# Kernel tuning notes

Hardware: AMD Instinct MI355X
Metric: run time of the kernel (lower is better)

Reference implementation:

```python
import jax, jax.numpy as jnp
import numpy as np

D_DIM = 100000  # vocabulary size
W_DIM = 128     # embedding width
BATCH = 4096    # number of (center, context) index pairs


def setup_inputs() -> dict:
    key = jax.random.key(0)
    k1, k2, kw1, kb1, kw2, kb2 = jax.random.split(key, 6)
    idx1 = jax.random.randint(k1, (BATCH,), 0, D_DIM, dtype=jnp.int64 if jax.config.jax_enable_x64 else jnp.int32)
    idx2 = jax.random.randint(k2, (BATCH,), 0, D_DIM, dtype=jnp.int64 if jax.config.jax_enable_x64 else jnp.int32)
    # torch.nn.Linear(D, W): weight [W, D], bias [W], uniform(-1/sqrt(D), 1/sqrt(D))
    bound = 1.0 / np.sqrt(D_DIM)
    W1 = jax.random.uniform(kw1, (W_DIM, D_DIM), jnp.float32, -bound, bound)
    b1 = jax.random.uniform(kb1, (W_DIM,), jnp.float32, -bound, bound)
    W2 = jax.random.uniform(kw2, (W_DIM, D_DIM), jnp.float32, -bound, bound)
    b2 = jax.random.uniform(kb2, (W_DIM,), jnp.float32, -bound, bound)
    return {"idx1": idx1, "idx2": idx2, "W1": W1, "b1": b1, "W2": W2, "b2": b2}


def reference(idx1, idx2, W1, b1, W2, b2):
    # Linear(one_hot(idx)) == weight[:, idx] + bias  -> direct row (column) gather.
    p1 = W1[:, idx1].T + b1              # [B, W_dim]
    p2 = W2[:, idx2].T + b2              # [B, W_dim]
    s = jax.nn.sigmoid(jnp.sum(p1 * p2, axis=-1))  # [B]
    # original: cat([1 - sigmoid, sigmoid]) -> [B, 2]
    return jnp.stack([1.0 - s, s], axis=-1)
```

## Files before the change

kernel.cpp:

```cpp
#include <hip/hip_runtime.h>
#include <math.h>

#define D_DIM 100000
#define W_DIM 128
#define BATCH 4096

__global__ __launch_bounds__(256) void sgns_kernel(
    const int* __restrict__ idx1,
    const int* __restrict__ idx2,
    const float* __restrict__ W1,
    const float* __restrict__ b1,
    const float* __restrict__ W2,
    const float* __restrict__ b2,
    float* __restrict__ out)
{
    const int gtid = blockIdx.x * blockDim.x + threadIdx.x;
    const int wave = gtid >> 6;
    const int lane = gtid & 63;
    if (wave >= BATCH) return;

    const int i1 = idx1[wave];
    const int i2 = idx2[wave];

    const int w0 = lane;
    const int w1 = lane + 64;

    const float a0 = W1[w0 * D_DIM + i1];
    const float a1 = W1[w1 * D_DIM + i1];
    const float c0 = W2[w0 * D_DIM + i2];
    const float c1 = W2[w1 * D_DIM + i2];

    const float p0 = a0 + b1[w0];
    const float p1 = a1 + b1[w1];
    const float q0 = c0 + b2[w0];
    const float q1 = c1 + b2[w1];

    float v = p0 * q0 + p1 * q1;

    #pragma unroll
    for (int off = 32; off > 0; off >>= 1)
        v += __shfl_down(v, off, 64);

    if (lane == 0) {
        const float s = 1.0f / (1.0f + expf(-v));
        out[wave * 2 + 0] = 1.0f - s;
        out[wave * 2 + 1] = s;
    }
}

extern "C" void kernel_launch(void* const* d_in, const int* in_sizes, int n_in,
                              void* d_out, int out_size, void* d_ws, size_t ws_size,
                              hipStream_t stream)
{
    const int*   idx1 = (const int*)  d_in[0];
    const int*   idx2 = (const int*)  d_in[1];
    const float* W1   = (const float*)d_in[2];
    const float* b1   = (const float*)d_in[3];
    const float* W2   = (const float*)d_in[4];
    const float* b2   = (const float*)d_in[5];
    float* out = (float*)d_out;

    const int threads = 256;
    const int blocks  = (BATCH * 64) / threads;
    sgns_kernel<<<blocks, threads, 0, stream>>>(idx1, idx2, W1, b1, W2, b2, out);
}
```

Baseline: 125.2 us.

## Gather embedding columns via inverse-index scatter so reads coalesce across vocabulary

Replaces the per-pair strided column gather with a four-kernel pipeline. It first initialises inverse-index maps, then uses atomicMin to map each vocabulary id to the first batch position that uses it. Next, threads indexed by vocabulary id copy the needed columns into compact row-major buffers, so adjacent threads read adjacent addresses. A final kernel computes the dot products from those buffers. This targets the uncoalesced 4-byte reads with 400KB stride, but adds three extra launches, workspace traffic, and a gather pass that scans all 100k ids per table.

```diff
diff --git a/kernel.cpp b/kernel.cpp
--- a/kernel.cpp
+++ b/kernel.cpp
@@ -4,38 +4,86 @@
 #define D_DIM 100000
 #define W_DIM 128
 #define BATCH 4096
+#define NOREP 0x7FFFFFFF
 
-__global__ __launch_bounds__(256) void sgns_kernel(
-    const int* __restrict__ idx1,
-    const int* __restrict__ idx2,
-    const float* __restrict__ W1,
-    const float* __restrict__ b1,
-    const float* __restrict__ W2,
-    const float* __restrict__ b2,
-    float* __restrict__ out)
+
+__global__ __launch_bounds__(256) void k_init(int* __restrict__ inv)
+{
+    const int t = blockIdx.x * 256 + threadIdx.x;
+    if (t < (2 * D_DIM) / 4)
+        reinterpret_cast<int4*>(inv)[t] = make_int4(NOREP, NOREP, NOREP, NOREP);
+}
+
+__global__ __launch_bounds__(256) void k_scatter(const int* __restrict__ idx1,
+                                                 const int* __restrict__ idx2,
+                                                 int* __restrict__ inv1,
+                                                 int* __restrict__ inv2)
+{
+    const int b = blockIdx.x * 256 + threadIdx.x;
+    if (b < BATCH) {
+        atomicMin(&inv1[idx1[b]], b);
+        atomicMin(&inv2[idx2[b]], b);
+    }
+}
+
+__global__ __launch_bounds__(256) void k_gather(const float* __restrict__ W1,
+                                                const float* __restrict__ W2,
+                                                const int*   __restrict__ inv1,
+                                                const int*   __restrict__ inv2,
+                                                float* __restrict__ p1,
+                                                float* __restrict__ p2)
+{
+    const float* __restrict__ W   = blockIdx.y ? W2   : W1;
+    const int*   __restrict__ inv = blockIdx.y ? inv2 : inv1;
+    float*       __restrict__ p   = blockIdx.y ? p2   : p1;
+
+    const int i = blockIdx.x * 256 + threadIdx.x;
+    if (i >= D_DIM) return;
+    const int j = inv[i];
+    if (j == NOREP) return;
+
+    const float* __restrict__ src = W + i;
+    float*       __restrict__ dst = p + j * W_DIM;
+    #pragma unroll 8
+    for (int w = 0; w < W_DIM; ++w)
+        dst[w] = src[w * D_DIM];
+}
+
+__global__ __launch_bounds__(256) void k_dot(const int* __restrict__ idx1,
+                                             const int* __restrict__ idx2,
+                                             const int* __restrict__ inv1,
+                                             const int* __restrict__ inv2,
+                                             const float* __restrict__ p1,
+                                             const float* __restrict__ p2,
+                                             const float* __restrict__ b1,
+                                             const float* __restrict__ b2,
+                                             float* __restrict__ out)
 {
     const int gtid = blockIdx.x * blockDim.x + threadIdx.x;
     const int wave = gtid >> 6;
     const int lane = gtid & 63;
     if (wave >= BATCH) return;
 
-    const int i1 = idx1[wave];
-    const int i2 = idx2[wave];
+    const int r1 = inv1[idx1[wave]];
+    const int r2 = inv2[idx2[wave]];
+
+    const float* __restrict__ P1 = p1 + r1 * W_DIM;
+    const float* __restrict__ P2 = p2 + r2 * W_DIM;
 
     const int w0 = lane;
     const int w1 = lane + 64;
 
-    const float a0 = W1[w0 * D_DIM + i1];
-    const float a1 = W1[w1 * D_DIM + i1];
-    const float c0 = W2[w0 * D_DIM + i2];
-    const float c1 = W2[w1 * D_DIM + i2];
+    const float a0 = P1[w0];
+    const float a1 = P1[w1];
+    const float c0 = P2[w0];
+    const float c1 = P2[w1];
 
-    const float p0 = a0 + b1[w0];
-    const float p1 = a1 + b1[w1];
-    const float q0 = c0 + b2[w0];
-    const float q1 = c1 + b2[w1];
+    const float x0 = a0 + b1[w0];
+    const float x1 = a1 + b1[w1];
+    const float y0 = c0 + b2[w0];
+    const float y1 = c1 + b2[w1];
 
-    float v = p0 * q0 + p1 * q1;
+    float v = x0 * y0 + x1 * y1;
 
     #pragma unroll
     for (int off = 32; off > 0; off >>= 1)
@@ -60,7 +108,28 @@
     const float* b2   = (const float*)d_in[5];
     float* out = (float*)d_out;
 
-    const int threads = 256;
-    const int blocks  = (BATCH * 64) / threads;
-    sgns_kernel<<<blocks, threads, 0, stream>>>(idx1, idx2, W1, b1, W2, b2, out);
+    char* ws = (char*)d_ws;
+    int*   inv1 = (int*)  (ws + 0);
+    int*   inv2 = (int*)  (ws + 400000);
+    float* p1   = (float*)(ws + 800000);
+    float* p2   = (float*)(ws + 2897152);
+
+    {
+        const int n_int4 = (2 * D_DIM) / 4;
+        const int blocks = (n_int4 + 255) / 256;
+        k_init<<<blocks, 256, 0, stream>>>(inv1);
+    }
+    {
+        const int blocks = (BATCH + 255) / 256;
+        k_scatter<<<blocks, 256, 0, stream>>>(idx1, idx2, inv1, inv2);
+    }
+    {
+        dim3 grid((D_DIM + 255) / 256, 2);
+        k_gather<<<grid, 256, 0, stream>>>(W1, W2, inv1, inv2, p1, p2);
+    }
+    {
+        const int blocks = (BATCH * 64) / 256;
+        k_dot<<<blocks, 256, 0, stream>>>(idx1, idx2, inv1, inv2,
+                                          p1, p2, b1, b2, out);
+    }
 }
```

Result: slower. 135.7 us (+8.3%).
